# Kernel tuning notes

Measured on AMD Instinct MI355X. Metric: run time of the kernel, lower is better.

Reference implementation:

```python
import jax, jax.numpy as jnp
import numpy as np

N, E = 10000, 320000
D, H, C = 256, 8, 32   # dim, heads, head_dim (dim//num_head)
DE, DF = 64, 1024      # edge_dim, dim_ff


def setup_inputs() -> dict:
    key = jax.random.key(0)
    ks = jax.random.split(key, 32)
    s = 0.05
    n = lambda k, shp: jax.random.normal(k, shp, jnp.float32) * s
    inp = {
        "nf": jax.random.normal(ks[0], (N, D), jnp.float32),
        "ei": jax.random.randint(ks[1], (2, E), 0, N),
        "ew": jax.random.normal(ks[2], (E, DE), jnp.float32),
        # GATConv 1
        "lin1": n(ks[3], (D, H * C)), "le1": n(ks[4], (DE, H * C)),
        "asrc1": n(ks[5], (H, C)), "adst1": n(ks[6], (H, C)), "aedge1": n(ks[7], (H, C)),
        "b1": jnp.zeros((H * C,), jnp.float32),
        # GATConv 2
        "lin2": n(ks[8], (D, H * C)), "le2": n(ks[9], (DE, H * C)),
        "asrc2": n(ks[10], (H, C)), "adst2": n(ks[11], (H, C)), "aedge2": n(ks[12], (H, C)),
        "b2": jnp.zeros((H * C,), jnp.float32),
        # LayerNorms
        "g1": jnp.ones((D,), jnp.float32), "be1": jnp.zeros((D,), jnp.float32),
        "g2": jnp.ones((D,), jnp.float32), "be2": jnp.zeros((D,), jnp.float32),
        "g3": jnp.ones((D,), jnp.float32), "be3": jnp.zeros((D,), jnp.float32),
        # FFN
        "w1": n(ks[13], (D, DF)), "fb1": jnp.zeros((DF,), jnp.float32),
        "w2": n(ks[14], (DF, D)), "fb2": jnp.zeros((D,), jnp.float32),
    }
    return inp


def _ln(x, g, b, eps=1e-6):
    # annotated-transformer LayerNorm: unbiased std, eps added to std
    mu = x.mean(-1, keepdims=True)
    sd = jnp.std(x, axis=-1, ddof=1, keepdims=True)
    return g * (x - mu) / (sd + eps) + b


def _gat(x, src, dst, ea, W, We, a_s, a_d, a_e, bias):
    # PyG GATConv with edge_dim, add_self_loops=True, fill_value='mean', concat=True
    ones = jnp.ones((src.shape[0], 1), x.dtype)
    cnt = jax.ops.segment_sum(ones, dst, num_segments=N)
    loop_attr = jax.ops.segment_sum(ea, dst, num_segments=N) / jnp.maximum(cnt, 1.0)
    idx = jnp.arange(N)
    srcf = jnp.concatenate([src, idx])
    dstf = jnp.concatenate([dst, idx])
    eaf = jnp.concatenate([ea, loop_attr], axis=0)          # [E+N, DE]
    xs = (x @ W).reshape(N, H, C)                            # [N,H,C]
    ef = (eaf @ We).reshape(-1, H, C)                        # [E+N,H,C]
    a_src = (xs * a_s).sum(-1)                               # [N,H]
    a_dst = (xs * a_d).sum(-1)                               # [N,H]
    alpha = a_src[srcf] + a_dst[dstf] + (ef * a_e).sum(-1)   # [E+N,H]
    alpha = jax.nn.leaky_relu(alpha, 0.2)
    m = jax.ops.segment_max(alpha, dstf, num_segments=N)     # segment softmax
    ex = jnp.exp(alpha - m[dstf])
    den = jax.ops.segment_sum(ex, dstf, num_segments=N)
    w = ex / (den[dstf] + 1e-16)                             # [E+N,H]
    out = jax.ops.segment_sum(w[:, :, None] * xs[srcf], dstf, num_segments=N)
    return out.reshape(N, H * C) + bias


def reference(nf, ei, ew, lin1, le1, asrc1, adst1, aedge1, b1,
              lin2, le2, asrc2, adst2, aedge2, b2,
              g1, be1, g2, be2, g3, be3, w1, fb1, w2, fb2):
    src, dst = ei[0], ei[1]
    h = _gat(nf, src, dst, ew, lin1, le1, asrc1, adst1, aedge1, b1)
    nf = nf + jax.nn.leaky_relu(_ln(h, g1, be1), 0.01)
    h = _gat(nf, src, dst, ew, lin2, le2, asrc2, adst2, aedge2, b2)
    nf = nf + jax.nn.leaky_relu(_ln(h, g2, be2), 0.01)
    h = jax.nn.relu(nf @ w1 + fb1) @ w2 + fb2
    nf = nf + jax.nn.leaky_relu(_ln(h, g3, be3), 0.01)
    return nf
```

## Files before the change

kernel.cpp:

```cpp
#include <hip/hip_runtime.h>
#include <hip/hip_bf16.h>
#include <math.h>

#define D 256
#define H 8
#define C 32
#define DE 64
#define DF 1024

static inline size_t align_up(size_t x, size_t a) { return (x + a - 1) / a * a; }

typedef __attribute__((ext_vector_type(8))) short short8;
typedef __attribute__((ext_vector_type(4))) float f32x4;

__device__ inline unsigned short f2b(float x) {
    __hip_bfloat16 h = __float2bfloat16(x);
    return *reinterpret_cast<unsigned short*>(&h);
}
__device__ inline float b2f(unsigned short u) {
    return __uint_as_float(((unsigned int)u) << 16);
}

__global__ void deg_kernel(const int* __restrict__ dst, int* __restrict__ deg, int E) {
    int e = blockIdx.x * 256 + threadIdx.x;
    if (e < E) atomicAdd(&deg[dst[e]], 1);
}

__global__ void partial_sum_kernel(const int* __restrict__ deg, int* __restrict__ part, int n) {
    int i = blockIdx.x * 256 + threadIdx.x;
    int v = (i < n) ? deg[i] : 0;
    for (int o = 1; o < 64; o <<= 1) v += __shfl_xor(v, o);
    __shared__ int w4[4];
    if ((threadIdx.x & 63) == 0) w4[threadIdx.x >> 6] = v;
    __syncthreads();
    if (threadIdx.x == 0) part[blockIdx.x] = w4[0] + w4[1] + w4[2] + w4[3];
}

__global__ void scan_part_kernel(int* __restrict__ part, int nb) {
    __shared__ int buf[256];
    int t = threadIdx.x;
    buf[t] = (t < nb) ? part[t] : 0;
    __syncthreads();
    for (int s = 1; s < 256; s <<= 1) {
        int v = (t >= s) ? buf[t - s] : 0;
        __syncthreads();
        buf[t] += v;
        __syncthreads();
    }
    int excl = (t == 0) ? 0 : buf[t - 1];
    if (t < nb) part[t] = excl;
}

__global__ void scan_final_kernel(const int* __restrict__ deg, const int* __restrict__ part,
                                  int* __restrict__ off, int* __restrict__ cursor, int n) {
    int b = blockIdx.x, t = threadIdx.x, i = b * 256 + t;
    __shared__ int buf[256];
    int v = (i < n) ? deg[i] : 0;
    buf[t] = v;
    __syncthreads();
    for (int s = 1; s < 256; s <<= 1) {
        int x = (t >= s) ? buf[t - s] : 0;
        __syncthreads();
        buf[t] += x;
        __syncthreads();
    }
    int excl = part[b] + buf[t] - v;
    if (i < n) { off[i] = excl; cursor[i] = excl; }
    if (i == n - 1) off[n] = excl + v;
}

__global__ void fill_kernel(const int* __restrict__ src, const int* __restrict__ dst,
                            int* __restrict__ cursor, int* __restrict__ eid,
                            int* __restrict__ src_csr, int E) {
    int e = blockIdx.x * 256 + threadIdx.x;
    if (e < E) {
        int p = atomicAdd(&cursor[dst[e]], 1);
        eid[p] = e;
        src_csr[p] = src[e];
    }
}

__global__ void prep_kernel(const float* __restrict__ lin1, const float* __restrict__ lin2,
                            const float* __restrict__ w1, const float* __restrict__ w2,
                            const float* __restrict__ le1, const float* __restrict__ ae1,
                            const float* __restrict__ le2, const float* __restrict__ ae2,
                            const float* __restrict__ nf0,
                            unsigned short* __restrict__ lin1T, unsigned short* __restrict__ lin2T,
                            unsigned short* __restrict__ w1T, unsigned short* __restrict__ w2T,
                            unsigned short* __restrict__ MeT, unsigned short* __restrict__ Abf,
                            size_t n_valid, size_t n_total) {
    int b = blockIdx.x;
    if (b > 640) {
        size_t i = ((size_t)(b - 641) * 256 + threadIdx.x) * 8;
        if (i >= n_total) return;
        ushort4 o0, o1;
        if (i < n_valid) {
            float4 a = *(const float4*)&nf0[i];
            float4 bb = *(const float4*)&nf0[i + 4];
            o0.x = f2b(a.x); o0.y = f2b(a.y); o0.z = f2b(a.z); o0.w = f2b(a.w);
            o1.x = f2b(bb.x); o1.y = f2b(bb.y); o1.z = f2b(bb.z); o1.w = f2b(bb.w);
        } else {
            o0.x = o0.y = o0.z = o0.w = 0;
            o1 = o0;
        }
        *(ushort4*)&Abf[i] = o0;
        *(ushort4*)&Abf[i + 4] = o1;
        return;
    }
    if (b == 640) {
        for (int t = threadIdx.x; t < 512; t += 256) {
            int d = t >> 3, h = t & 7;
            float s1 = 0.f, s2 = 0.f;
            for (int c = 0; c < C; ++c) {
                s1 += le1[d * (H * C) + h * C + c] * ae1[h * C + c];
                s2 += le2[d * (H * C) + h * C + c] * ae2[h * C + c];
            }
            MeT[h * 64 + d] = f2b(s1);
            MeT[(8 + h) * 64 + d] = f2b(s2);
        }
        return;
    }
    __shared__ float tile[32][33];
    const float* in; unsigned short* outp; int K, N, tt;
    if (b < 64)       { in = lin1; outp = lin1T; K = D;  N = D;  tt = b; }
    else if (b < 128) { in = lin2; outp = lin2T; K = D;  N = D;  tt = b - 64; }
    else if (b < 384) { in = w1;   outp = w1T;   K = D;  N = DF; tt = b - 128; }
    else              { in = w2;   outp = w2T;   K = DF; N = D;  tt = b - 384; }
    int ntn = N >> 5;
    int bn = (tt % ntn) * 32, bk = (tt / ntn) * 32;
    int tx = threadIdx.x & 31, ty = threadIdx.x >> 5;
    for (int i = ty; i < 32; i += 8)
        tile[i][tx] = in[(size_t)(bk + i) * N + bn + tx];
    __syncthreads();
    for (int i = ty; i < 32; i += 8)
        outp[(size_t)(bn + i) * K + bk + tx] = f2b(tile[tx][i]);
}

template<int BM>
__global__ __launch_bounds__(256) void mfma_gemm_kernel(
    const unsigned short* __restrict__ A, const unsigned short* __restrict__ BT,
    const float* __restrict__ bias, float* __restrict__ Cf, unsigned short* __restrict__ Cb,
    int M, int Nc, int K, int relu,
    const float* __restrict__ a_s, const float* __restrict__ a_d,
    float* __restrict__ asrcO, float* __restrict__ adstO) {
    constexpr int NR = (BM == 128) ? 4 : 2;
    constexpr int AI = BM / 32;
    __shared__ unsigned short As[BM * 64];
    __shared__ unsigned short Bs[128 * 64];
    int t = threadIdx.x;
    int lane = t & 63, w = t >> 6;
    int gm0 = blockIdx.x * BM, gn0 = blockIdx.y * 128;
    f32x4 acc[4][NR] = {};
    int srow = lane >> 3, scol = (lane & 7) * 8;
    int wm = (BM == 128) ? (w >> 1) * 64 : 0;
    int wn = (BM == 128) ? (w & 1) * 64 : w * 32;
    int fr = lane & 15, fk = (lane >> 4) * 8;

    for (int k0 = 0; k0 < K; k0 += 64) {
        __syncthreads();
#pragma unroll
        for (int i = 0; i < AI; ++i) {
            int rb = w * (8 * AI) + i * 8;
            const unsigned short* ga = A + (size_t)(gm0 + rb + srow) * K + k0 + scol;
            __builtin_amdgcn_global_load_lds(
                (const __attribute__((address_space(1))) unsigned int*)ga,
                (__attribute__((address_space(3))) unsigned int*)&As[rb * 64], 16, 0, 0);
        }
#pragma unroll
        for (int i = 0; i < 4; ++i) {
            int rb = w * 32 + i * 8;
            const unsigned short* gb = BT + (size_t)(gn0 + rb + srow) * K + k0 + scol;
            __builtin_amdgcn_global_load_lds(
                (const __attribute__((address_space(1))) unsigned int*)gb,
                (__attribute__((address_space(3))) unsigned int*)&Bs[rb * 64], 16, 0, 0);
        }
        __syncthreads();
#pragma unroll
        for (int kk = 0; kk < 64; kk += 32) {
            short8 a[4], b[NR];
#pragma unroll
            for (int m = 0; m < 4; ++m)
                a[m] = *(const short8*)&As[(wm + m * 16 + fr) * 64 + kk + fk];
#pragma unroll
            for (int n = 0; n < NR; ++n)
                b[n] = *(const short8*)&Bs[(wn + n * 16 + fr) * 64 + kk + fk];
#pragma unroll
            for (int m = 0; m < 4; ++m)
#pragma unroll
                for (int n = 0; n < NR; ++n)
                    acc[m][n] = __builtin_amdgcn_mfma_f32_16x16x32_bf16(a[m], b[n], acc[m][n], 0, 0, 0);
        }
    }
    int fcol = lane & 15, frow4 = (lane >> 4) * 4;
#pragma unroll
    for (int m = 0; m < 4; ++m) {
#pragma unroll
        for (int i = 0; i < 4; ++i) {
            int gr = gm0 + wm + m * 16 + frow4 + i;
            if (gr >= M) continue;
#pragma unroll
            for (int n = 0; n < NR; ++n) {
                int gc = gn0 + wn + n * 16 + fcol;
                float v = acc[m][n][i];
                if (bias) v += bias[gc];
                if (relu) v = fmaxf(v, 0.f);
                if (Cb) Cb[(size_t)gr * Nc + gc] = f2b(v);
                else    Cf[(size_t)gr * Nc + gc] = v;
            }
        }
    }
    if (BM == 64 && a_s) {
        int head = (gn0 >> 5) + w;
        float as0 = a_s[head * 32 + fcol], as1 = a_s[head * 32 + 16 + fcol];
        float ad0 = a_d[head * 32 + fcol], ad1 = a_d[head * 32 + 16 + fcol];
#pragma unroll
        for (int m = 0; m < 4; ++m) {
#pragma unroll
            for (int i = 0; i < 4; ++i) {
                float vs = acc[m][0][i] * as0 + acc[m][1][i] * as1;
                float vd = acc[m][0][i] * ad0 + acc[m][1][i] * ad1;
#pragma unroll
                for (int o = 1; o < 16; o <<= 1) {
                    vs += __shfl_xor(vs, o);
                    vd += __shfl_xor(vd, o);
                }
                int r = gm0 + m * 16 + frow4 + i;
                if (fcol == 0 && r < M) {
                    asrcO[r * 8 + head] = vs;
                    adstO[r * 8 + head] = vd;
                }
            }
        }
    }
}

__global__ __launch_bounds__(256) void ffn2_ln_kernel(
    const unsigned short* __restrict__ A, const unsigned short* __restrict__ BT,
    const float* __restrict__ bias, const float* __restrict__ nf_in,
    const float* __restrict__ gamma, const float* __restrict__ beta,
    float* __restrict__ out, int M) {
    __shared__ unsigned short As[64 * 64];
    __shared__ unsigned short Bs[256 * 64];
    __shared__ float redS1[4][64], redS2[4][64];
    __shared__ float muS[64], invS[64];
    int t = threadIdx.x, lane = t & 63, w = t >> 6;
    int gm0 = blockIdx.x * 64;
    f32x4 acc[4][4] = {};
    int srow = lane >> 3, scol = (lane & 7) * 8;
    int wn = w * 64;
    int fr = lane & 15, fk = (lane >> 4) * 8;
    for (int k0 = 0; k0 < DF; k0 += 64) {
        __syncthreads();
#pragma unroll
        for (int i = 0; i < 2; ++i) {
            int rb = w * 16 + i * 8;
            const unsigned short* ga = A + (size_t)(gm0 + rb + srow) * DF + k0 + scol;
            __builtin_amdgcn_global_load_lds(
                (const __attribute__((address_space(1))) unsigned int*)ga,
                (__attribute__((address_space(3))) unsigned int*)&As[rb * 64], 16, 0, 0);
        }
#pragma unroll
        for (int i = 0; i < 8; ++i) {
            int rb = w * 64 + i * 8;
            const unsigned short* gb = BT + (size_t)(rb + srow) * DF + k0 + scol;
            __builtin_amdgcn_global_load_lds(
                (const __attribute__((address_space(1))) unsigned int*)gb,
                (__attribute__((address_space(3))) unsigned int*)&Bs[rb * 64], 16, 0, 0);
        }
        __syncthreads();
#pragma unroll
        for (int kk = 0; kk < 64; kk += 32) {
            short8 a[4], b[4];
#pragma unroll
            for (int m = 0; m < 4; ++m)
                a[m] = *(const short8*)&As[(m * 16 + fr) * 64 + kk + fk];
#pragma unroll
            for (int n = 0; n < 4; ++n)
                b[n] = *(const short8*)&Bs[(wn + n * 16 + fr) * 64 + kk + fk];
#pragma unroll
            for (int m = 0; m < 4; ++m)
#pragma unroll
                for (int n = 0; n < 4; ++n)
                    acc[m][n] = __builtin_amdgcn_mfma_f32_16x16x32_bf16(a[m], b[n], acc[m][n], 0, 0, 0);
        }
    }
    int fcol = lane & 15, frow4 = (lane >> 4) * 4;
#pragma unroll
    for (int m = 0; m < 4; ++m) {
#pragma unroll
        for (int i = 0; i < 4; ++i) {
            float vs1 = 0.f, vs2 = 0.f;
#pragma unroll
            for (int n = 0; n < 4; ++n) {
                float vv = acc[m][n][i] + bias[wn + n * 16 + fcol];
                acc[m][n][i] = vv;
                vs1 += vv; vs2 += vv * vv;
            }
#pragma unroll
            for (int o = 1; o < 16; o <<= 1) {
                vs1 += __shfl_xor(vs1, o);
                vs2 += __shfl_xor(vs2, o);
            }
            if (fcol == 0) {
                redS1[w][m * 16 + frow4 + i] = vs1;
                redS2[w][m * 16 + frow4 + i] = vs2;
            }
        }
    }
    __syncthreads();
    if (t < 64) {
        float s1 = redS1[0][t] + redS1[1][t] + redS1[2][t] + redS1[3][t];
        float s2 = redS2[0][t] + redS2[1][t] + redS2[2][t] + redS2[3][t];
        float mu = s1 / 256.f;
        float var = fmaxf((s2 - 256.f * mu * mu) / 255.f, 0.f);
        muS[t] = mu;
        invS[t] = 1.f / (sqrtf(var) + 1e-6f);
    }
    __syncthreads();
#pragma unroll
    for (int m = 0; m < 4; ++m) {
#pragma unroll
        for (int i = 0; i < 4; ++i) {
            int r = m * 16 + frow4 + i;
            int gr = gm0 + r;
            if (gr >= M) continue;
            float mu = muS[r], inv = invS[r];
#pragma unroll
            for (int n = 0; n < 4; ++n) {
                int gc = wn + n * 16 + fcol;
                float y = gamma[gc] * (acc[m][n][i] - mu) * inv + beta[gc];
                y = y > 0.f ? y : 0.01f * y;
                out[(size_t)gr * D + gc] = nf_in[(size_t)gr * D + gc] + y;
            }
        }
    }
}

__global__ __launch_bounds__(256) void ealpha_mfma_kernel(
    const float* __restrict__ ew, const int* __restrict__ eid,
    const unsigned short* __restrict__ MeT,
    float* __restrict__ eA1c, float* __restrict__ eA2c, int E) {
    int t = threadIdx.x;
    int lane = t & 63, w = t >> 6;
    int p0 = blockIdx.x * 64 + w * 16;
    int r = lane & 15, g = lane >> 4;
    int pr = p0 + r; if (pr > E - 1) pr = E - 1;
    int er = eid[pr];
    const float* rowp = ew + (size_t)er * DE;
    float4 x0 = *(const float4*)&rowp[g * 8];
    float4 x1 = *(const float4*)&rowp[g * 8 + 4];
    float4 y0 = *(const float4*)&rowp[32 + g * 8];
    float4 y1 = *(const float4*)&rowp[32 + g * 8 + 4];
    short8 a0, a1;
    a0[0] = (short)f2b(x0.x); a0[1] = (short)f2b(x0.y); a0[2] = (short)f2b(x0.z); a0[3] = (short)f2b(x0.w);
    a0[4] = (short)f2b(x1.x); a0[5] = (short)f2b(x1.y); a0[6] = (short)f2b(x1.z); a0[7] = (short)f2b(x1.w);
    a1[0] = (short)f2b(y0.x); a1[1] = (short)f2b(y0.y); a1[2] = (short)f2b(y0.z); a1[3] = (short)f2b(y0.w);
    a1[4] = (short)f2b(y1.x); a1[5] = (short)f2b(y1.y); a1[6] = (short)f2b(y1.z); a1[7] = (short)f2b(y1.w);
    short8 b0 = *(const short8*)&MeT[r * 64 + g * 8];
    short8 b1 = *(const short8*)&MeT[r * 64 + 32 + g * 8];
    f32x4 acc = {};
    acc = __builtin_amdgcn_mfma_f32_16x16x32_bf16(a0, b0, acc, 0, 0, 0);
    acc = __builtin_amdgcn_mfma_f32_16x16x32_bf16(a1, b1, acc, 0, 0, 0);
#pragma unroll
    for (int i = 0; i < 4; ++i) {
        int p = p0 + g * 4 + i;
        if (p < E) {
            if (r < 8) eA1c[(size_t)p * 8 + r] = acc[i];
            else       eA2c[(size_t)p * 8 + (r - 8)] = acc[i];
        }
    }
}

__global__ __launch_bounds__(256) void gat_node_kernel(
    const int* __restrict__ off, const int* __restrict__ src_csr,
    const float* __restrict__ eAc,
    const float* __restrict__ asrc, const float* __restrict__ adst,
    const unsigned short* __restrict__ xsb, const float* __restrict__ nf_in,
    const float* __restrict__ bias, const float* __restrict__ gamma,
    const float* __restrict__ beta, float* __restrict__ nf_out,
    unsigned short* __restrict__ nf_out_b, int N) {
    int lane = threadIdx.x & 63;
    int n = blockIdx.x * 4 + (threadIdx.x >> 6);
    if (n >= N) return;
    int e0 = off[n], e1 = off[n + 1], deg = e1 - e0;
    int h = lane & 7;
    int hw = lane >> 3;

    float adstn = adst[n * 8 + h];
    float asn = asrc[n * 8 + h];

    float acc0 = 0.f, acc1 = 0.f, acc2 = 0.f, acc3 = 0.f;
    float den0 = 0.f, easum = 0.f;
    int nb8 = (deg + 7) >> 3;

#define LOAD_SE(b, S, EA, A) { A = ((b) * 8 + hw) < deg; int sp_ = e0 + (b) * 8 + hw; \
    S = A ? src_csr[sp_] : n; EA = A ? eAc[(size_t)sp_ * 8 + h] : 0.f; }

    if (nb8 > 0) {
        int s0, s1, s2; float ea0, ea1, ea2; bool a0, a1, a2;
        LOAD_SE(0, s0, ea0, a0);
        LOAD_SE(1, s1, ea1, a1);
        LOAD_SE(2, s2, ea2, a2);
        float as0 = a0 ? asrc[s0 * 8 + h] : 0.f;
        float as1 = a1 ? asrc[s1 * 8 + h] : 0.f;
        ushort4 uA[8], uB[8];
#pragma unroll
        for (int kk = 0; kk < 8; ++kk) {
            int sk = __shfl(s0, kk * 8 + hw);
            uA[kk] = *(const ushort4*)&xsb[(size_t)sk * D + lane * 4];
        }
        int it = 0;
        while (true) {
            if (it + 1 < nb8) {
#pragma unroll
                for (int kk = 0; kk < 8; ++kk) {
                    int sk = __shfl(s1, kk * 8 + hw);
                    uB[kk] = *(const ushort4*)&xsb[(size_t)sk * D + lane * 4];
                }
            }
            {
                float as2 = a2 ? asrc[s2 * 8 + h] : 0.f;
                int s3; float ea3; bool a3;
                LOAD_SE(it + 3, s3, ea3, a3);
                float al = as0 + adstn + ea0;
                al = al > 0.f ? al : 0.2f * al;
                float ex = a0 ? expf(al) : 0.f;
                den0 += ex; easum += ea0;
#pragma unroll
                for (int kk = 0; kk < 8; ++kk) {
                    float exk = __shfl(ex, kk * 8 + hw);
                    acc0 = fmaf(exk, b2f(uA[kk].x), acc0);
                    acc1 = fmaf(exk, b2f(uA[kk].y), acc1);
                    acc2 = fmaf(exk, b2f(uA[kk].z), acc2);
                    acc3 = fmaf(exk, b2f(uA[kk].w), acc3);
                }
                s0 = s1; ea0 = ea1; as0 = as1; a0 = a1;
                s1 = s2; ea1 = ea2; as1 = as2; a1 = a2;
                s2 = s3; ea2 = ea3; a2 = a3;
            }
            if (++it >= nb8) break;
            if (it + 1 < nb8) {
#pragma unroll
                for (int kk = 0; kk < 8; ++kk) {
                    int sk = __shfl(s1, kk * 8 + hw);
                    uA[kk] = *(const ushort4*)&xsb[(size_t)sk * D + lane * 4];
                }
            }
            {
                float as2 = a2 ? asrc[s2 * 8 + h] : 0.f;
                int s3; float ea3; bool a3;
                LOAD_SE(it + 3, s3, ea3, a3);
                float al = as0 + adstn + ea0;
                al = al > 0.f ? al : 0.2f * al;
                float ex = a0 ? expf(al) : 0.f;
                den0 += ex; easum += ea0;
#pragma unroll
                for (int kk = 0; kk < 8; ++kk) {
                    float exk = __shfl(ex, kk * 8 + hw);
                    acc0 = fmaf(exk, b2f(uB[kk].x), acc0);
                    acc1 = fmaf(exk, b2f(uB[kk].y), acc1);
                    acc2 = fmaf(exk, b2f(uB[kk].z), acc2);
                    acc3 = fmaf(exk, b2f(uB[kk].w), acc3);
                }
                s0 = s1; ea0 = ea1; as0 = as1; a0 = a1;
                s1 = s2; ea1 = ea2; as1 = as2; a1 = a2;
                s2 = s3; ea2 = ea3; a2 = a3;
            }
            if (++it >= nb8) break;
        }
    }
#undef LOAD_SE
    den0  += __shfl_xor(den0, 8);
    den0  += __shfl_xor(den0, 16);
    den0  += __shfl_xor(den0, 32);
    easum += __shfl_xor(easum, 8);
    easum += __shfl_xor(easum, 16);
    easum += __shfl_xor(easum, 32);
    float sa = easum / (float)(deg > 0 ? deg : 1);
    float als = asn + adstn + sa;
    als = als > 0.f ? als : 0.2f * als;
    float exSelf = expf(als);
    {
        float exs = __shfl(exSelf, hw);
        ushort4 u = *(const ushort4*)&xsb[(size_t)n * D + lane * 4];
        acc0 = fmaf(exs, b2f(u.x), acc0);
        acc1 = fmaf(exs, b2f(u.y), acc1);
        acc2 = fmaf(exs, b2f(u.z), acc2);
        acc3 = fmaf(exs, b2f(u.w), acc3);
    }
    den0 += exSelf;
    float denOwn = __shfl(den0, hw);
    float inv = 1.f / (denOwn + 1e-16f);

    int t0 = lane * 4;
    float4 bi = *(const float4*)&bias[t0];
    float o0 = acc0 * inv + bi.x;
    float o1 = acc1 * inv + bi.y;
    float o2 = acc2 * inv + bi.z;
    float o3 = acc3 * inv + bi.w;

    float s1r = o0 + o1 + o2 + o3;
    float s2r = o0 * o0 + o1 * o1 + o2 * o2 + o3 * o3;
    for (int o = 1; o < 64; o <<= 1) { s1r += __shfl_xor(s1r, o); s2r += __shfl_xor(s2r, o); }
    float mu = s1r / 256.f;
    float var = fmaxf((s2r - 256.f * mu * mu) / 255.f, 0.f);
    float sdv = sqrtf(var) + 1e-6f;
    float4 ga = *(const float4*)&gamma[t0];
    float4 be = *(const float4*)&beta[t0];
    float4 nin = *(const float4*)&nf_in[(size_t)n * D + t0];
    float y0 = ga.x * (o0 - mu) / sdv + be.x; y0 = y0 > 0.f ? y0 : 0.01f * y0;
    float y1 = ga.y * (o1 - mu) / sdv + be.y; y1 = y1 > 0.f ? y1 : 0.01f * y1;
    float y2 = ga.z * (o2 - mu) / sdv + be.z; y2 = y2 > 0.f ? y2 : 0.01f * y2;
    float y3 = ga.w * (o3 - mu) / sdv + be.w; y3 = y3 > 0.f ? y3 : 0.01f * y3;
    float r0 = nin.x + y0, r1 = nin.y + y1, r2 = nin.z + y2, r3 = nin.w + y3;
    float4 outv; outv.x = r0; outv.y = r1; outv.z = r2; outv.w = r3;
    *(float4*)&nf_out[(size_t)n * D + t0] = outv;
    ushort4 ob; ob.x = f2b(r0); ob.y = f2b(r1); ob.z = f2b(r2); ob.w = f2b(r3);
    *(ushort4*)&nf_out_b[(size_t)n * D + t0] = ob;
}

extern "C" void kernel_launch(void* const* d_in, const int* in_sizes, int n_in,
                              void* d_out, int out_size, void* d_ws, size_t ws_size,
                              hipStream_t stream) {
    const float* nf0    = (const float*)d_in[0];
    const int*   ei     = (const int*)d_in[1];
    const float* ew     = (const float*)d_in[2];
    const float* lin1   = (const float*)d_in[3];
    const float* le1    = (const float*)d_in[4];
    const float* asrc1w = (const float*)d_in[5];
    const float* adst1w = (const float*)d_in[6];
    const float* aedge1 = (const float*)d_in[7];
    const float* b1     = (const float*)d_in[8];
    const float* lin2   = (const float*)d_in[9];
    const float* le2    = (const float*)d_in[10];
    const float* asrc2w = (const float*)d_in[11];
    const float* adst2w = (const float*)d_in[12];
    const float* aedge2 = (const float*)d_in[13];
    const float* b2     = (const float*)d_in[14];
    const float* g1     = (const float*)d_in[15];
    const float* be1    = (const float*)d_in[16];
    const float* g2     = (const float*)d_in[17];
    const float* be2    = (const float*)d_in[18];
    const float* g3     = (const float*)d_in[19];
    const float* be3    = (const float*)d_in[20];
    const float* w1     = (const float*)d_in[21];
    const float* fb1    = (const float*)d_in[22];
    const float* w2     = (const float*)d_in[23];
    const float* fb2    = (const float*)d_in[24];

    const int N = in_sizes[0] / D;
    const int E = in_sizes[1] / 2;
    const int Mpad = ((N + 127) / 128) * 128;
    const int* srcI = ei;
    const int* dstI = ei + E;

    char* ws = (char*)d_ws;
    size_t ob = 0;
    auto alloc = [&](size_t bytes) { void* p = ws + ob; ob = align_up(ob + bytes, 256); return p; };
    int*   deg     = (int*)alloc((size_t)N * 4);
    int*   csr_off = (int*)alloc((size_t)(N + 1) * 4);
    int*   cursor  = (int*)alloc((size_t)N * 4);
    int*   part    = (int*)alloc(1024);
    int*   eid     = (int*)alloc((size_t)E * 4);
    int*   src_csr = (int*)alloc((size_t)E * 4);
    unsigned short* MeT = (unsigned short*)alloc(16 * 64 * 2);
    float* asrcB   = (float*)alloc((size_t)N * H * 4);
    float* adstB   = (float*)alloc((size_t)N * H * 4);
    float* eA1c    = (float*)alloc((size_t)E * H * 4);
    float* eA2c    = (float*)alloc((size_t)E * H * 4);
    float* nfw     = (float*)alloc((size_t)N * D * 4);
    unsigned short* xs_b  = (unsigned short*)alloc((size_t)Mpad * D * 2);
    unsigned short* Abf   = (unsigned short*)alloc((size_t)Mpad * D * 2);
    unsigned short* lin1T = (unsigned short*)alloc((size_t)D * D * 2);
    unsigned short* lin2T = (unsigned short*)alloc((size_t)D * D * 2);
    unsigned short* w1T   = (unsigned short*)alloc((size_t)DF * D * 2);
    unsigned short* w2T   = (unsigned short*)alloc((size_t)D * DF * 2);
    unsigned short* hidden = (unsigned short*)ws;
    (void)ws_size;
    float* out = (float*)d_out;

    hipMemsetAsync(deg, 0, (size_t)N * 4, stream);

    int eb = (E + 255) / 256;
    int nb = (N + 255) / 256;
    deg_kernel<<<eb, 256, 0, stream>>>(dstI, deg, E);
    partial_sum_kernel<<<nb, 256, 0, stream>>>(deg, part, N);
    scan_part_kernel<<<1, 256, 0, stream>>>(part, nb);
    scan_final_kernel<<<nb, 256, 0, stream>>>(deg, part, csr_off, cursor, N);
    fill_kernel<<<eb, 256, 0, stream>>>(srcI, dstI, cursor, eid, src_csr, E);

    const size_t nvalid = (size_t)N * D, ntot = (size_t)Mpad * D;
    int cb = (int)((ntot / 8 + 255) / 256);
    prep_kernel<<<641 + cb, 256, 0, stream>>>(lin1, lin2, w1, w2, le1, aedge1, le2, aedge2, nf0,
                                              lin1T, lin2T, w1T, w2T, MeT, Abf, nvalid, ntot);
    ealpha_mfma_kernel<<<(E + 63) / 64, 256, 0, stream>>>(ew, eid, MeT, eA1c, eA2c, E);

    int gatb = (N + 3) / 4;

    mfma_gemm_kernel<64><<<dim3(Mpad / 64, 2), 256, 0, stream>>>(
        Abf, lin1T, nullptr, nullptr, xs_b, N, D, D, 0, asrc1w, adst1w, asrcB, adstB);
    gat_node_kernel<<<gatb, 256, 0, stream>>>(csr_off, src_csr, eA1c, asrcB, adstB,
                                              xs_b, nf0, b1, g1, be1, nfw, Abf, N);
    mfma_gemm_kernel<64><<<dim3(Mpad / 64, 2), 256, 0, stream>>>(
        Abf, lin2T, nullptr, nullptr, xs_b, N, D, D, 0, asrc2w, adst2w, asrcB, adstB);
    gat_node_kernel<<<gatb, 256, 0, stream>>>(csr_off, src_csr, eA2c, asrcB, adstB,
                                              xs_b, nfw, b2, g2, be2, nfw, Abf, N);
    mfma_gemm_kernel<128><<<dim3(Mpad / 128, 8), 256, 0, stream>>>(
        Abf, w1T, fb1, nullptr, hidden, Mpad, DF, D, 1, nullptr, nullptr, nullptr, nullptr);
    ffn2_ln_kernel<<<(N + 63) / 64, 256, 0, stream>>>(hidden, w2T, fb2, nfw, g3, be3, out, N);
}
```

Baseline: 238.4 us.

## Merge preprocessing launches: fold degree count, scan, and edge-alpha into neighbours

Folds the degree-counting atomics into the weight-prep kernel as extra blocks. The scan_part kernel is removed; each scan_final block now serially sums the preceding block partials. The edge-alpha MFMA kernel and the first layer-1 projection GEMM are merged into one launch that dispatches on block index. This removes three kernel launches and their serialization gaps, and lets independent work share one grid. The cost is a small serial loop in thread 0 of each scan block and heterogeneous blocks within the fused kernels.

```diff
diff --git a/kernel.cpp b/kernel.cpp
--- a/kernel.cpp
+++ b/kernel.cpp
@@ -21,75 +21,22 @@
     return __uint_as_float(((unsigned int)u) << 16);
 }
 
-__global__ void deg_kernel(const int* __restrict__ dst, int* __restrict__ deg, int E) {
-    int e = blockIdx.x * 256 + threadIdx.x;
-    if (e < E) atomicAdd(&deg[dst[e]], 1);
-}
-
-__global__ void partial_sum_kernel(const int* __restrict__ deg, int* __restrict__ part, int n) {
-    int i = blockIdx.x * 256 + threadIdx.x;
-    int v = (i < n) ? deg[i] : 0;
-    for (int o = 1; o < 64; o <<= 1) v += __shfl_xor(v, o);
-    __shared__ int w4[4];
-    if ((threadIdx.x & 63) == 0) w4[threadIdx.x >> 6] = v;
-    __syncthreads();
-    if (threadIdx.x == 0) part[blockIdx.x] = w4[0] + w4[1] + w4[2] + w4[3];
-}
-
-__global__ void scan_part_kernel(int* __restrict__ part, int nb) {
-    __shared__ int buf[256];
-    int t = threadIdx.x;
-    buf[t] = (t < nb) ? part[t] : 0;
-    __syncthreads();
-    for (int s = 1; s < 256; s <<= 1) {
-        int v = (t >= s) ? buf[t - s] : 0;
-        __syncthreads();
-        buf[t] += v;
-        __syncthreads();
-    }
-    int excl = (t == 0) ? 0 : buf[t - 1];
-    if (t < nb) part[t] = excl;
-}
-
-__global__ void scan_final_kernel(const int* __restrict__ deg, const int* __restrict__ part,
-                                  int* __restrict__ off, int* __restrict__ cursor, int n) {
-    int b = blockIdx.x, t = threadIdx.x, i = b * 256 + t;
-    __shared__ int buf[256];
-    int v = (i < n) ? deg[i] : 0;
-    buf[t] = v;
-    __syncthreads();
-    for (int s = 1; s < 256; s <<= 1) {
-        int x = (t >= s) ? buf[t - s] : 0;
-        __syncthreads();
-        buf[t] += x;
-        __syncthreads();
-    }
-    int excl = part[b] + buf[t] - v;
-    if (i < n) { off[i] = excl; cursor[i] = excl; }
-    if (i == n - 1) off[n] = excl + v;
-}
-
-__global__ void fill_kernel(const int* __restrict__ src, const int* __restrict__ dst,
-                            int* __restrict__ cursor, int* __restrict__ eid,
-                            int* __restrict__ src_csr, int E) {
-    int e = blockIdx.x * 256 + threadIdx.x;
-    if (e < E) {
-        int p = atomicAdd(&cursor[dst[e]], 1);
-        eid[p] = e;
-        src_csr[p] = src[e];
-    }
-}
-
-__global__ void prep_kernel(const float* __restrict__ lin1, const float* __restrict__ lin2,
-                            const float* __restrict__ w1, const float* __restrict__ w2,
-                            const float* __restrict__ le1, const float* __restrict__ ae1,
-                            const float* __restrict__ le2, const float* __restrict__ ae2,
-                            const float* __restrict__ nf0,
-                            unsigned short* __restrict__ lin1T, unsigned short* __restrict__ lin2T,
-                            unsigned short* __restrict__ w1T, unsigned short* __restrict__ w2T,
-                            unsigned short* __restrict__ MeT, unsigned short* __restrict__ Abf,
-                            size_t n_valid, size_t n_total) {
+__global__ void prep_deg_kernel(const float* __restrict__ lin1, const float* __restrict__ lin2,
+                                const float* __restrict__ w1, const float* __restrict__ w2,
+                                const float* __restrict__ le1, const float* __restrict__ ae1,
+                                const float* __restrict__ le2, const float* __restrict__ ae2,
+                                const float* __restrict__ nf0, const int* __restrict__ dst,
+                                unsigned short* __restrict__ lin1T, unsigned short* __restrict__ lin2T,
+                                unsigned short* __restrict__ w1T, unsigned short* __restrict__ w2T,
+                                unsigned short* __restrict__ MeT, unsigned short* __restrict__ Abf,
+                                int* __restrict__ deg,
+                                size_t n_valid, size_t n_total, int cb, int E) {
     int b = blockIdx.x;
+    if (b >= 641 + cb) {
+        int e = (b - 641 - cb) * 256 + threadIdx.x;
+        if (e < E) atomicAdd(&deg[dst[e]], 1);
+        return;
+    }
     if (b > 640) {
         size_t i = ((size_t)(b - 641) * 256 + threadIdx.x) * 8;
         if (i >= n_total) return;
@@ -134,6 +81,51 @@
     __syncthreads();
     for (int i = ty; i < 32; i += 8)
         outp[(size_t)(bn + i) * K + bk + tx] = f2b(tile[tx][i]);
+}
+
+__global__ void partial_sum_kernel(const int* __restrict__ deg, int* __restrict__ part, int n) {
+    int i = blockIdx.x * 256 + threadIdx.x;
+    int v = (i < n) ? deg[i] : 0;
+    for (int o = 1; o < 64; o <<= 1) v += __shfl_xor(v, o);
+    __shared__ int w4[4];
+    if ((threadIdx.x & 63) == 0) w4[threadIdx.x >> 6] = v;
+    __syncthreads();
+    if (threadIdx.x == 0) part[blockIdx.x] = w4[0] + w4[1] + w4[2] + w4[3];
+}
+
+__global__ void scan_final_kernel(const int* __restrict__ deg, const int* __restrict__ part,
+                                  int* __restrict__ off, int* __restrict__ cursor, int n) {
+    int b = blockIdx.x, t = threadIdx.x, i = b * 256 + t;
+    __shared__ int buf[256];
+    __shared__ int baseS;
+    if (t == 0) {
+        int base = 0;
+        for (int j = 0; j < b; ++j) base += part[j];
+        baseS = base;
+    }
+    int v = (i < n) ? deg[i] : 0;
+    buf[t] = v;
+    __syncthreads();
+    for (int s = 1; s < 256; s <<= 1) {
+        int x = (t >= s) ? buf[t - s] : 0;
+        __syncthreads();
+        buf[t] += x;
+        __syncthreads();
+    }
+    int excl = baseS + buf[t] - v;
+    if (i < n) { off[i] = excl; cursor[i] = excl; }
+    if (i == n - 1) off[n] = excl + v;
+}
+
+__global__ void fill_kernel(const int* __restrict__ src, const int* __restrict__ dst,
+                            int* __restrict__ cursor, int* __restrict__ eid,
+                            int* __restrict__ src_csr, int E) {
+    int e = blockIdx.x * 256 + threadIdx.x;
+    if (e < E) {
+        int p = atomicAdd(&cursor[dst[e]], 1);
+        eid[p] = e;
+        src_csr[p] = src[e];
+    }
 }
 
 template<int BM>
@@ -234,6 +226,131 @@
     }
 }
 
+__global__ __launch_bounds__(256) void fused_ea_gemm1_kernel(
+    const float* __restrict__ ew, const int* __restrict__ eid,
+    const unsigned short* __restrict__ MeT,
+    float* __restrict__ eA1c, float* __restrict__ eA2c, int E, int EAB,
+    const unsigned short* __restrict__ A, const unsigned short* __restrict__ BT,
+    unsigned short* __restrict__ Cb, int M, int nbx,
+    const float* __restrict__ a_s, const float* __restrict__ a_d,
+    float* __restrict__ asrcO, float* __restrict__ adstO) {
+    __shared__ unsigned short As[64 * 64];
+    __shared__ unsigned short Bs[128 * 64];
+    int t = threadIdx.x;
+    int lane = t & 63, w = t >> 6;
+
+    if ((int)blockIdx.x < EAB) {
+        int p0 = blockIdx.x * 64 + w * 16;
+        int r = lane & 15, g = lane >> 4;
+        int pr = p0 + r; if (pr > E - 1) pr = E - 1;
+        int er = eid[pr];
+        const float* rowp = ew + (size_t)er * DE;
+        float4 x0 = *(const float4*)&rowp[g * 8];
+        float4 x1 = *(const float4*)&rowp[g * 8 + 4];
+        float4 y0 = *(const float4*)&rowp[32 + g * 8];
+        float4 y1 = *(const float4*)&rowp[32 + g * 8 + 4];
+        short8 a0, a1;
+        a0[0] = (short)f2b(x0.x); a0[1] = (short)f2b(x0.y); a0[2] = (short)f2b(x0.z); a0[3] = (short)f2b(x0.w);
+        a0[4] = (short)f2b(x1.x); a0[5] = (short)f2b(x1.y); a0[6] = (short)f2b(x1.z); a0[7] = (short)f2b(x1.w);
+        a1[0] = (short)f2b(y0.x); a1[1] = (short)f2b(y0.y); a1[2] = (short)f2b(y0.z); a1[3] = (short)f2b(y0.w);
+        a1[4] = (short)f2b(y1.x); a1[5] = (short)f2b(y1.y); a1[6] = (short)f2b(y1.z); a1[7] = (short)f2b(y1.w);
+        short8 b0 = *(const short8*)&MeT[r * 64 + g * 8];
+        short8 b1 = *(const short8*)&MeT[r * 64 + 32 + g * 8];
+        f32x4 acc = {};
+        acc = __builtin_amdgcn_mfma_f32_16x16x32_bf16(a0, b0, acc, 0, 0, 0);
+        acc = __builtin_amdgcn_mfma_f32_16x16x32_bf16(a1, b1, acc, 0, 0, 0);
+#pragma unroll
+        for (int i = 0; i < 4; ++i) {
+            int p = p0 + g * 4 + i;
+            if (p < E) {
+                if (r < 8) eA1c[(size_t)p * 8 + r] = acc[i];
+                else       eA2c[(size_t)p * 8 + (r - 8)] = acc[i];
+            }
+        }
+        return;
+    }
+    int id = blockIdx.x - EAB;
+    int bx = id % nbx, by = id / nbx;
+    int gm0 = bx * 64, gn0 = by * 128;
+    f32x4 acc[4][2] = {};
+    int srow = lane >> 3, scol = (lane & 7) * 8;
+    int wn = w * 32;
+    int fr = lane & 15, fk = (lane >> 4) * 8;
+
+    for (int k0 = 0; k0 < D; k0 += 64) {
+        __syncthreads();
+#pragma unroll
+        for (int i = 0; i < 2; ++i) {
+            int rb = w * 16 + i * 8;
+            const unsigned short* ga = A + (size_t)(gm0 + rb + srow) * D + k0 + scol;
+            __builtin_amdgcn_global_load_lds(
+                (const __attribute__((address_space(1))) unsigned int*)ga,
+                (__attribute__((address_space(3))) unsigned int*)&As[rb * 64], 16, 0, 0);
+        }
+#pragma unroll
+        for (int i = 0; i < 4; ++i) {
+            int rb = w * 32 + i * 8;
+            const unsigned short* gb = BT + (size_t)(gn0 + rb + srow) * D + k0 + scol;
+            __builtin_amdgcn_global_load_lds(
+                (const __attribute__((address_space(1))) unsigned int*)gb,
+                (__attribute__((address_space(3))) unsigned int*)&Bs[rb * 64], 16, 0, 0);
+        }
+        __syncthreads();
+#pragma unroll
+        for (int kk = 0; kk < 64; kk += 32) {
+            short8 a[4], b[2];
+#pragma unroll
+            for (int m = 0; m < 4; ++m)
+                a[m] = *(const short8*)&As[(m * 16 + fr) * 64 + kk + fk];
+#pragma unroll
+            for (int n = 0; n < 2; ++n)
+                b[n] = *(const short8*)&Bs[(wn + n * 16 + fr) * 64 + kk + fk];
+#pragma unroll
+            for (int m = 0; m < 4; ++m)
+#pragma unroll
+                for (int n = 0; n < 2; ++n)
+                    acc[m][n] = __builtin_amdgcn_mfma_f32_16x16x32_bf16(a[m], b[n], acc[m][n], 0, 0, 0);
+        }
+    }
+    int fcol = lane & 15, frow4 = (lane >> 4) * 4;
+#pragma unroll
+    for (int m = 0; m < 4; ++m) {
+#pragma unroll
+        for (int i = 0; i < 4; ++i) {
+            int gr = gm0 + m * 16 + frow4 + i;
+            if (gr >= M) continue;
+#pragma unroll
+            for (int n = 0; n < 2; ++n) {
+                int gc = gn0 + wn + n * 16 + fcol;
+                Cb[(size_t)gr * D + gc] = f2b(acc[m][n][i]);
+            }
+        }
+    }
+    {
+        int head = (gn0 >> 5) + w;
+        float as0 = a_s[head * 32 + fcol], as1 = a_s[head * 32 + 16 + fcol];
+        float ad0 = a_d[head * 32 + fcol], ad1 = a_d[head * 32 + 16 + fcol];
+#pragma unroll
+        for (int m = 0; m < 4; ++m) {
+#pragma unroll
+            for (int i = 0; i < 4; ++i) {
+                float vs = acc[m][0][i] * as0 + acc[m][1][i] * as1;
+                float vd = acc[m][0][i] * ad0 + acc[m][1][i] * ad1;
+#pragma unroll
+                for (int o = 1; o < 16; o <<= 1) {
+                    vs += __shfl_xor(vs, o);
+                    vd += __shfl_xor(vd, o);
+                }
+                int r = gm0 + m * 16 + frow4 + i;
+                if (fcol == 0 && r < M) {
+                    asrcO[r * 8 + head] = vs;
+                    adstO[r * 8 + head] = vd;
+                }
+            }
+        }
+    }
+}
+
 __global__ __launch_bounds__(256) void ffn2_ln_kernel(
     const unsigned short* __restrict__ A, const unsigned short* __restrict__ BT,
     const float* __restrict__ bias, const float* __restrict__ nf_in,
@@ -332,41 +449,6 @@
                 y = y > 0.f ? y : 0.01f * y;
                 out[(size_t)gr * D + gc] = nf_in[(size_t)gr * D + gc] + y;
             }
-        }
-    }
-}
-
-__global__ __launch_bounds__(256) void ealpha_mfma_kernel(
-    const float* __restrict__ ew, const int* __restrict__ eid,
-    const unsigned short* __restrict__ MeT,
-    float* __restrict__ eA1c, float* __restrict__ eA2c, int E) {
-    int t = threadIdx.x;
-    int lane = t & 63, w = t >> 6;
-    int p0 = blockIdx.x * 64 + w * 16;
-    int r = lane & 15, g = lane >> 4;
-    int pr = p0 + r; if (pr > E - 1) pr = E - 1;
-    int er = eid[pr];
-    const float* rowp = ew + (size_t)er * DE;
-    float4 x0 = *(const float4*)&rowp[g * 8];
-    float4 x1 = *(const float4*)&rowp[g * 8 + 4];
-    float4 y0 = *(const float4*)&rowp[32 + g * 8];
-    float4 y1 = *(const float4*)&rowp[32 + g * 8 + 4];
-    short8 a0, a1;
-    a0[0] = (short)f2b(x0.x); a0[1] = (short)f2b(x0.y); a0[2] = (short)f2b(x0.z); a0[3] = (short)f2b(x0.w);
-    a0[4] = (short)f2b(x1.x); a0[5] = (short)f2b(x1.y); a0[6] = (short)f2b(x1.z); a0[7] = (short)f2b(x1.w);
-    a1[0] = (short)f2b(y0.x); a1[1] = (short)f2b(y0.y); a1[2] = (short)f2b(y0.z); a1[3] = (short)f2b(y0.w);
-    a1[4] = (short)f2b(y1.x); a1[5] = (short)f2b(y1.y); a1[6] = (short)f2b(y1.z); a1[7] = (short)f2b(y1.w);
-    short8 b0 = *(const short8*)&MeT[r * 64 + g * 8];
-    short8 b1 = *(const short8*)&MeT[r * 64 + 32 + g * 8];
-    f32x4 acc = {};
-    acc = __builtin_amdgcn_mfma_f32_16x16x32_bf16(a0, b0, acc, 0, 0, 0);
-    acc = __builtin_amdgcn_mfma_f32_16x16x32_bf16(a1, b1, acc, 0, 0, 0);
-#pragma unroll
-    for (int i = 0; i < 4; ++i) {
-        int p = p0 + g * 4 + i;
-        if (p < E) {
-            if (r < 8) eA1c[(size_t)p * 8 + r] = acc[i];
-            else       eA2c[(size_t)p * 8 + (r - 8)] = acc[i];
         }
     }
 }
@@ -583,25 +665,26 @@
 
     int eb = (E + 255) / 256;
     int nb = (N + 255) / 256;
-    deg_kernel<<<eb, 256, 0, stream>>>(dstI, deg, E);
+    const size_t nvalid = (size_t)N * D, ntot = (size_t)Mpad * D;
+    int cb = (int)((ntot / 8 + 255) / 256);
+
+    prep_deg_kernel<<<641 + cb + eb, 256, 0, stream>>>(
+        lin1, lin2, w1, w2, le1, aedge1, le2, aedge2, nf0, dstI,
+        lin1T, lin2T, w1T, w2T, MeT, Abf, deg, nvalid, ntot, cb, E);
     partial_sum_kernel<<<nb, 256, 0, stream>>>(deg, part, N);
-    scan_part_kernel<<<1, 256, 0, stream>>>(part, nb);
     scan_final_kernel<<<nb, 256, 0, stream>>>(deg, part, csr_off, cursor, N);
     fill_kernel<<<eb, 256, 0, stream>>>(srcI, dstI, cursor, eid, src_csr, E);
 
-    const size_t nvalid = (size_t)N * D, ntot = (size_t)Mpad * D;
-    int cb = (int)((ntot / 8 + 255) / 256);
-    prep_kernel<<<641 + cb, 256, 0, stream>>>(lin1, lin2, w1, w2, le1, aedge1, le2, aedge2, nf0,
-                                              lin1T, lin2T, w1T, w2T, MeT, Abf, nvalid, ntot);
-    ealpha_mfma_kernel<<<(E + 63) / 64, 256, 0, stream>>>(ew, eid, MeT, eA1c, eA2c, E);
-
+    int EAB = (E + 63) / 64;
+    int nbx = Mpad / 64;
     int gatb = (N + 3) / 4;
 
-    mfma_gemm_kernel<64><<<dim3(Mpad / 64, 2), 256, 0, stream>>>(
-        Abf, lin1T, nullptr, nullptr, xs_b, N, D, D, 0, asrc1w, adst1w, asrcB, adstB);
+    fused_ea_gemm1_kernel<<<EAB + nbx * 2, 256, 0, stream>>>(
+        ew, eid, MeT, eA1c, eA2c, E, EAB,
+        Abf, lin1T, xs_b, N, nbx, asrc1w, adst1w, asrcB, adstB);
     gat_node_kernel<<<gatb, 256, 0, stream>>>(csr_off, src_csr, eA1c, asrcB, adstB,
                                               xs_b, nf0, b1, g1, be1, nfw, Abf, N);
-    mfma_gemm_kernel<64><<<dim3(Mpad / 64, 2), 256, 0, stream>>>(
+    mfma_gemm_kernel<64><<<dim3(nbx, 2), 256, 0, stream>>>(
         Abf, lin2T, nullptr, nullptr, xs_b, N, D, D, 0, asrc2w, adst2w, asrcB, adstB);
     gat_node_kernel<<<gatb, 256, 0, stream>>>(csr_off, src_csr, eA2c, asrcB, adstB,
                                               xs_b, nfw, b2, g2, be2, nfw, Abf, N);
```

New measurement: 228.9 us. -4.0%, faster.
